# Kernel optimization log

Measured on AMD Instinct MI355X. Metric: run time of the kernel, lower is better.

The kernel has to match this reference:

```python
import jax, jax.numpy as jnp
import numpy as np

# Topology constants for size='large'
S = 490          # total switches: 128+64+64+96+64+32+32+10
W = 64           # n_wavelengths
M = 32           # n_modes
PS = 4           # patch_size
NPATCH = 49      # 7x7 patches of a 28x28 image
V1_START = 0
OUT_START = 480  # OUT region = last 10 switches
OUT_COUNT = 10
N_CLASSES = 10
SAT = 1.0        # cfg.saturation (not shown in source; standard value)
DECAY = 0.15
EPS = 1e-8


def encode_batch(images):
    """Real-valued patch encoding: [B,28,28] -> [B,49,64,32]."""
    B = images.shape[0]
    # unfold into non-overlapping 4x4 patches
    p = images[:, :7 * PS, :7 * PS].reshape(B, 7, PS, 7, PS)
    p = p.transpose(0, 1, 3, 2, 4).reshape(B, NPATCH, PS * PS)
    p = jnp.pad(p, ((0, 0), (0, 0), (0, M - PS * PS)))  # pad 16 -> 32 modes
    w_idx = jnp.arange(W, dtype=jnp.float32)
    w_weights = 1.0 - jnp.abs(w_idx - 32.0) / 64.0      # [W]
    return p[:, :, None, :] * w_weights[None, None, :, None]  # [B,NP,W,M]


def setup_inputs() -> dict:
    key = jax.random.key(0)
    k = jax.random.split(key, 7)
    images = jax.random.uniform(k[0], (8, 28, 28), dtype=jnp.float32)
    connectivity = jax.random.normal(k[1], (S, S), dtype=jnp.float32) * 0.05
    wavelength_weights = jax.random.uniform(k[2], (S, W), dtype=jnp.float32)
    switch_gain = jax.random.normal(k[3], (S,), dtype=jnp.float32) * 0.1
    switch_bias = jax.random.normal(k[4], (S,), dtype=jnp.float32) * 0.1
    readout_w = jax.random.normal(k[5], (N_CLASSES, OUT_COUNT), dtype=jnp.float32) * 0.1
    readout_b = jnp.zeros((N_CLASSES,), dtype=jnp.float32)
    return {
        "images": images,
        "connectivity": connectivity,
        "wavelength_weights": wavelength_weights,
        "switch_gain": switch_gain,
        "switch_bias": switch_bias,
        "readout_w": readout_w,
        "readout_b": readout_b,
        "n_steps": 15,
        "injection_steps": 5,
    }


def reference(images, connectivity, wavelength_weights, switch_gain, switch_bias,
              readout_w, readout_b, n_steps, injection_steps):
    B = images.shape[0]
    enc = encode_batch(images)                          # [B,49,W,M]
    enc_max = jnp.max(jnp.abs(enc))
    enc = jnp.where(enc_max > EPS, enc / enc_max, enc)
    inj = enc * 0.3                                     # injected signal (real; imag part is 0)

    gain = jax.nn.softplus(switch_gain)[None, :, None, None]
    bias = switch_bias[None, :, None, None]
    ww = wavelength_weights[None, :, :, None]

    field = jnp.zeros((B, S, W, M), jnp.float32)
    output = jnp.zeros((B, S, W, M), jnp.float32)

    def step(carry, t):
        field, output = carry
        # injection into V1 (min(v1_count=128, 49 patches) = 49) for t < injection_steps
        gate = jnp.where(t < injection_steps, 1.0, 0.0).astype(jnp.float32)
        field = field.at[:, V1_START:V1_START + NPATCH].add(gate * inj)
        # network step (complex magnitudes; imag is identically 0)
        out_mag = jnp.sqrt(output * output + EPS)
        gathered = jax.nn.relu(jnp.einsum('bswm,st->btwm', out_mag, connectivity))
        field_mag = jnp.sqrt(field * field + EPS) * (1.0 - DECAY) + gathered * 0.25
        weighted = field_mag * ww
        activated = SAT * jnp.tanh((weighted * gain + bias) / SAT)
        return (field_mag, activated), None

    (field, output), _ = jax.lax.scan(step, (field, output), jnp.arange(n_steps))

    out_field = output[:, OUT_START:OUT_START + OUT_COUNT]       # [B,10,W,M]
    out_energy = (out_field * out_field + EPS).sum(axis=(2, 3))  # [B,10]
    out_features = jnp.log1p(out_energy + EPS)
    return out_features @ readout_w.T + readout_b
```

## Files before the change

kernel.cpp:

```cpp
#include <hip/hip_runtime.h>
#include <math.h>

#define S_DIM 490
#define NPATCH 49
#define EPSF 1e-8f
#define SP 512
#define CI 8192
#define CPB 32
#define NBLK 256
#define HEAVY0 252
#define OMS 520

typedef __attribute__((ext_vector_type(8))) short bf16x8;
typedef __attribute__((ext_vector_type(4))) float f32x4;

__device__ __forceinline__ unsigned short f2bf(float x) {
    unsigned int u = __float_as_uint(x);
    unsigned int r = (u + 0x7FFF + ((u >> 16) & 1)) >> 16;
    return (unsigned short)r;
}
__device__ __forceinline__ float bf2f(unsigned short u) {
    return __uint_as_float(((unsigned int)u) << 16);
}

__global__ void k_max(const float* __restrict__ img, float* __restrict__ encmax) {
    __shared__ float red[256];
    float m = 0.f;
    for (int i = threadIdx.x; i < 8 * 28 * 28; i += 256)
        m = fmaxf(m, fabsf(img[i]));
    red[threadIdx.x] = m;
    __syncthreads();
    for (int s = 128; s > 0; s >>= 1) {
        if (threadIdx.x < s) red[threadIdx.x] = fmaxf(red[threadIdx.x], red[threadIdx.x + s]);
        __syncthreads();
    }
    if (threadIdx.x == 0) *encmax = red[0];
}

__global__ void k_prep(const float* __restrict__ ww, const float* __restrict__ sg,
                       const float* __restrict__ sb, float* __restrict__ K1,
                       float* __restrict__ K2) {
    int i = blockIdx.x * 256 + threadIdx.x;
    if (i < 64 * SP) {
        int w = i >> 9, t = i & (SP - 1);
        K1[i] = (t < S_DIM) ? ww[t * 64 + w] * log1pf(expf(sg[t])) : 0.f;
    }
    if (i < SP) K2[i] = (i < S_DIM) ? sb[i] : 0.f;
}

__global__ void k_connP(const float* __restrict__ conn, unsigned short* __restrict__ connP) {
    int i = blockIdx.x * 256 + threadIdx.x;
    int j    = i & 7;
    int lane = (i >> 3) & 63;
    int k    = (i >> 9) & 15;
    int tt   = (i >> 13) & 1;
    int strip = i >> 14;
    int t = strip * 32 + tt * 16 + (lane & 15);
    int s = k * 32 + (lane >> 4) * 8 + j;
    float v = (t < S_DIM && s < S_DIM) ? conn[s * S_DIM + t] : 0.f;
    connP[i] = f2bf(v);
}

__global__ void k_inj(const float* __restrict__ img, const float* __restrict__ encmax,
                      float* __restrict__ injT) {
    int i = blockIdx.x * 256 + threadIdx.x;
    int c = i >> 6, tt = i & 63;
    int b = c >> 10, w = (c >> 4) & 63, m = c & 15;
    float em = *encmax;
    float scale = (em > EPSF) ? (0.3f / em) : 0.3f;
    float v = 0.f;
    if (tt < NPATCH) {
        int r = (tt / 7) * 4 + (m >> 2);
        int col = (tt % 7) * 4 + (m & 3);
        float wgt = 1.0f - fabsf((float)w - 32.0f) * (1.0f / 64.0f);
        v = img[(b * 28 + r) * 28 + col] * wgt * scale;
    }
    injT[i] = v;
}

#define MFMA(A, B, C) __builtin_amdgcn_mfma_f32_16x16x32_bf16(A, B, C, 0, 0, 0)

__global__ __launch_bounds__(1024, 4) void k_run(
    const unsigned short* __restrict__ connP, const float* __restrict__ injT,
    const float* __restrict__ K1, const float* __restrict__ K2,
    const int* __restrict__ injSteps, float* __restrict__ partials,
    float* __restrict__ partialsS)
{
    __shared__ unsigned short om[48 * OMS];
    const int bk   = blockIdx.x;
    const int tid  = threadIdx.x;
    const int wv   = tid >> 6;
    const int lane = tid & 63;
    const int l16  = lane & 15, lq = lane >> 4;
    const bool heavy = (bk >= HEAVY0);
    const int c0 = bk * CPB;

    {
        const unsigned short iv = f2bf(1e-4f);
        for (int i = tid; i < 48 * OMS; i += 1024) om[i] = iv;
    }

    const int nInj = injSteps[0];
    const unsigned short* aP = connP + (size_t)(wv * 32) * 512 + lane * 8;

    f32x4 k1r[2][2], k2r[2], k1h[2];
    #pragma unroll
    for (int tt = 0; tt < 2; ++tt) {
        int t0 = (wv << 5) + tt * 16 + lq * 4;
        k2r[tt] = *(const f32x4*)(K2 + t0);
        #pragma unroll
        for (int cc = 0; cc < 2; ++cc) {
            int w = (2 * bk + cc) & 63;
            k1r[tt][cc] = *(const f32x4*)(K1 + w * SP + t0);
        }
        if (heavy) {
            int wsh = (bk - HEAVY0) * 16 + l16;
            k1h[tt] = *(const f32x4*)(K1 + wsh * SP + t0);
        }
    }

    const int rb0 = l16 * OMS;
    const int rb1 = (16 + l16) * OMS;
    const int rb2 = (32 + l16) * OMS;

    f32x4 fld[2][2] = {};
    f32x4 fld2[2] = {};
    __syncthreads();

    for (int st = 0; st < 15; ++st) {
        f32x4 acc[2][2] = {};
        f32x4 acc2[2] = {};
        __builtin_amdgcn_s_setprio(1);
        #pragma unroll 4
        for (int k = 0; k < 16; ++k) {
            bf16x8 a0 = *(const bf16x8*)(aP + (size_t)(k)      * 512);
            bf16x8 a1 = *(const bf16x8*)(aP + (size_t)(16 + k) * 512);
            int sOff = k * 32 + lq * 8;
            bf16x8 b0 = *(const bf16x8*)&om[rb0 + sOff];
            bf16x8 b1 = *(const bf16x8*)&om[rb1 + sOff];
            acc[0][0] = MFMA(a0, b0, acc[0][0]);
            acc[0][1] = MFMA(a0, b1, acc[0][1]);
            acc[1][0] = MFMA(a1, b0, acc[1][0]);
            acc[1][1] = MFMA(a1, b1, acc[1][1]);
            if (heavy) {
                bf16x8 b2 = *(const bf16x8*)&om[rb2 + sOff];
                acc2[0] = MFMA(a0, b2, acc2[0]);
                acc2[1] = MFMA(a1, b2, acc2[1]);
            }
        }
        __builtin_amdgcn_s_setprio(0);
        __syncthreads();

        const bool injNow = (wv < 2) && (st < nInj);
        #pragma unroll
        for (int tt = 0; tt < 2; ++tt) {
            int t0 = (wv << 5) + tt * 16 + lq * 4;
            f32x4 k2 = k2r[tt];
            #pragma unroll
            for (int cc = 0; cc < 2; ++cc) {
                int cg = c0 + cc * 16 + l16;
                f32x4 k1 = k1r[tt][cc];
                f32x4 f = fld[tt][cc];
                if (injNow) f += *(const f32x4*)(injT + (size_t)cg * 64 + t0);
                f32x4 ac = acc[tt][cc];
                float o_[4];
                #pragma unroll
                for (int r = 0; r < 4; ++r) {
                    float g  = fmaxf(ac[r], 0.f);
                    float fm = fabsf(f[r]) * 0.85f + 0.25f * g;
                    float x  = fabsf(fm * k1[r] + k2[r]);
                    float e  = exp2f(x * 2.8853900817779268f);
                    o_[r] = 1.f - 2.f * __builtin_amdgcn_rcpf(e + 1.f);
                    f[r] = fm;
                }
                fld[tt][cc] = f;
                unsigned int r01, r23;
                asm("v_cvt_pk_bf16_f32 %0, %1, %2" : "=v"(r01) : "v"(o_[0]), "v"(o_[1]));
                asm("v_cvt_pk_bf16_f32 %0, %1, %2" : "=v"(r23) : "v"(o_[2]), "v"(o_[3]));
                int cl = cc * 16 + l16;
                *(uint2*)&om[cl * OMS + t0] = make_uint2(r01, r23);
            }
            if (heavy) {
                f32x4 k1 = k1h[tt];
                f32x4 fh = fld2[tt];
                f32x4 ah = acc2[tt];
                float oh[4];
                #pragma unroll
                for (int r = 0; r < 4; ++r) {
                    float g  = fmaxf(ah[r], 0.f);
                    float fm = fabsf(fh[r]) * 0.85f + 0.25f * g;
                    float x  = fabsf(fm * k1[r] + k2[r]);
                    float e  = exp2f(x * 2.8853900817779268f);
                    oh[r] = 1.f - 2.f * __builtin_amdgcn_rcpf(e + 1.f);
                    fh[r] = fm;
                }
                fld2[tt] = fh;
                unsigned int h01, h23;
                asm("v_cvt_pk_bf16_f32 %0, %1, %2" : "=v"(h01) : "v"(oh[0]), "v"(oh[1]));
                asm("v_cvt_pk_bf16_f32 %0, %1, %2" : "=v"(h23) : "v"(oh[2]), "v"(oh[3]));
                *(uint2*)&om[(32 + l16) * OMS + t0] = make_uint2(h01, h23);
            }
        }
        __syncthreads();
    }

    if (wv == 0) {
        int cl = (lane < 48) ? lane : 0;
        #pragma unroll
        for (int o = 0; o < 10; ++o) {
            float v = bf2f(om[cl * OMS + 480 + o]);
            float e = v * v;
            float em = (lane < 32) ? e : 0.f;
            em += __shfl_xor(em, 1);  em += __shfl_xor(em, 2);
            em += __shfl_xor(em, 4);  em += __shfl_xor(em, 8);
            em += __shfl_xor(em, 16);
            if (lane == 0) partials[bk * 10 + o] = em;
            if (heavy) {
                float es = (lane >= 32 && lane < 48) ? e : 0.f;
                es += __shfl_xor(es, 1); es += __shfl_xor(es, 2);
                es += __shfl_xor(es, 4); es += __shfl_xor(es, 8);
                if (lane == 32) partialsS[(bk - HEAVY0) * 10 + o] = es;
            }
        }
    }
}

__global__ void k_fin(const float* __restrict__ partials, const float* __restrict__ partialsS,
                      const float* __restrict__ rw, const float* __restrict__ rb,
                      float* __restrict__ out) {
    __shared__ float fe[80];
    int tid = threadIdx.x;
    if (tid < 80) {
        int b = tid / 10, o = tid % 10;
        float e = 0.f;
        #pragma unroll 8
        for (int j = 0; j < 32; ++j) e += partials[(b * 32 + j) * 10 + o];
        float es = 0.f;
        #pragma unroll
        for (int j = 0; j < 4; ++j) es += partialsS[j * 10 + o];
        e += 16.f * es + 2048.f * EPSF;
        fe[tid] = log1pf(e + EPSF);
    }
    __syncthreads();
    if (tid < 80) {
        int b = tid / 10, cls = tid % 10;
        float a = rb[cls];
        #pragma unroll
        for (int k = 0; k < 10; ++k) a += fe[b * 10 + k] * rw[cls * 10 + k];
        out[tid] = a;
    }
}

extern "C" void kernel_launch(void* const* d_in, const int* in_sizes, int n_in,
                              void* d_out, int out_size, void* d_ws, size_t ws_size,
                              hipStream_t stream) {
    (void)in_sizes; (void)n_in; (void)out_size; (void)ws_size;
    const float* img   = (const float*)d_in[0];
    const float* conn  = (const float*)d_in[1];
    const float* ww    = (const float*)d_in[2];
    const float* sgain = (const float*)d_in[3];
    const float* sbias = (const float*)d_in[4];
    const float* rw    = (const float*)d_in[5];
    const float* rb    = (const float*)d_in[6];
    const int* injsteps = (const int*)d_in[8];

    char* w = (char*)d_ws;
    unsigned short* connP = (unsigned short*)w;
    float* injT = (float*)(w + (size_t)SP * SP * 2);
    float* K1   = injT + (size_t)CI * 64;
    float* K2   = K1 + 64 * SP;
    float* encmax    = K2 + SP;
    float* partials  = encmax + 4;
    float* partialsS = partials + NBLK * 10;

    k_max  <<<1, 256, 0, stream>>>(img, encmax);
    k_prep <<<128, 256, 0, stream>>>(ww, sgain, sbias, K1, K2);
    k_connP<<<(SP * SP) / 256, 256, 0, stream>>>(conn, connP);
    k_inj  <<<(CI * 64) / 256, 256, 0, stream>>>(img, encmax, injT);

    k_run<<<NBLK, 1024, 0, stream>>>(connP, injT, K1, K2, injsteps, partials, partialsS);
    k_fin<<<1, 128, 0, stream>>>(partials, partialsS, rw, rb, (float*)d_out);
}
```

Before: 135.7 us.

## Double-buffer LDS state to drop a barrier and preload half of connectivity

Doubles the shared output buffer so each step reads one buffer and writes the other, which removes the barrier between the MFMA phase and the activation phase. It also keeps the first eight k-slices of the connectivity A-operand in registers across all steps, avoiding repeated global loads for them. In exchange, LDS use and VGPR pressure both roughly double, which risks spills or lower occupancy.

```diff
diff --git a/kernel.cpp b/kernel.cpp
--- a/kernel.cpp
+++ b/kernel.cpp
@@ -86,7 +86,7 @@
     const int* __restrict__ injSteps, float* __restrict__ partials,
     float* __restrict__ partialsS)
 {
-    __shared__ unsigned short om[48 * OMS];
+    __shared__ unsigned short om[2][48 * OMS];
     const int bk   = blockIdx.x;
     const int tid  = threadIdx.x;
     const int wv   = tid >> 6;
@@ -97,11 +97,18 @@
 
     {
         const unsigned short iv = f2bf(1e-4f);
-        for (int i = tid; i < 48 * OMS; i += 1024) om[i] = iv;
+        for (int i = tid; i < 2 * 48 * OMS; i += 1024) ((unsigned short*)om)[i] = iv;
     }
 
     const int nInj = injSteps[0];
     const unsigned short* aP = connP + (size_t)(wv * 32) * 512 + lane * 8;
+
+    bf16x8 pa0[8], pa1[8];
+    #pragma unroll
+    for (int k = 0; k < 8; ++k) {
+        pa0[k] = *(const bf16x8*)(aP + (size_t)(k)      * 512);
+        pa1[k] = *(const bf16x8*)(aP + (size_t)(16 + k) * 512);
+    }
 
     f32x4 k1r[2][2], k2r[2], k1h[2];
     #pragma unroll
@@ -128,28 +135,44 @@
     __syncthreads();
 
     for (int st = 0; st < 15; ++st) {
+        const unsigned short* bufR = om[st & 1];
+        unsigned short* bufW = om[(st + 1) & 1];
         f32x4 acc[2][2] = {};
         f32x4 acc2[2] = {};
         __builtin_amdgcn_s_setprio(1);
-        #pragma unroll 4
-        for (int k = 0; k < 16; ++k) {
+        #pragma unroll
+        for (int k = 0; k < 8; ++k) {
+            int sOff = k * 32 + lq * 8;
+            bf16x8 b0 = *(const bf16x8*)&bufR[rb0 + sOff];
+            bf16x8 b1 = *(const bf16x8*)&bufR[rb1 + sOff];
+            acc[0][0] = MFMA(pa0[k], b0, acc[0][0]);
+            acc[0][1] = MFMA(pa0[k], b1, acc[0][1]);
+            acc[1][0] = MFMA(pa1[k], b0, acc[1][0]);
+            acc[1][1] = MFMA(pa1[k], b1, acc[1][1]);
+            if (heavy) {
+                bf16x8 b2 = *(const bf16x8*)&bufR[rb2 + sOff];
+                acc2[0] = MFMA(pa0[k], b2, acc2[0]);
+                acc2[1] = MFMA(pa1[k], b2, acc2[1]);
+            }
+        }
+        #pragma unroll
+        for (int k = 8; k < 16; ++k) {
             bf16x8 a0 = *(const bf16x8*)(aP + (size_t)(k)      * 512);
             bf16x8 a1 = *(const bf16x8*)(aP + (size_t)(16 + k) * 512);
             int sOff = k * 32 + lq * 8;
-            bf16x8 b0 = *(const bf16x8*)&om[rb0 + sOff];
-            bf16x8 b1 = *(const bf16x8*)&om[rb1 + sOff];
+            bf16x8 b0 = *(const bf16x8*)&bufR[rb0 + sOff];
+            bf16x8 b1 = *(const bf16x8*)&bufR[rb1 + sOff];
             acc[0][0] = MFMA(a0, b0, acc[0][0]);
             acc[0][1] = MFMA(a0, b1, acc[0][1]);
             acc[1][0] = MFMA(a1, b0, acc[1][0]);
             acc[1][1] = MFMA(a1, b1, acc[1][1]);
             if (heavy) {
-                bf16x8 b2 = *(const bf16x8*)&om[rb2 + sOff];
+                bf16x8 b2 = *(const bf16x8*)&bufR[rb2 + sOff];
                 acc2[0] = MFMA(a0, b2, acc2[0]);
                 acc2[1] = MFMA(a1, b2, acc2[1]);
             }
         }
         __builtin_amdgcn_s_setprio(0);
-        __syncthreads();
 
         const bool injNow = (wv < 2) && (st < nInj);
         #pragma unroll
@@ -178,7 +201,7 @@
                 asm("v_cvt_pk_bf16_f32 %0, %1, %2" : "=v"(r01) : "v"(o_[0]), "v"(o_[1]));
                 asm("v_cvt_pk_bf16_f32 %0, %1, %2" : "=v"(r23) : "v"(o_[2]), "v"(o_[3]));
                 int cl = cc * 16 + l16;
-                *(uint2*)&om[cl * OMS + t0] = make_uint2(r01, r23);
+                *(uint2*)&bufW[cl * OMS + t0] = make_uint2(r01, r23);
             }
             if (heavy) {
                 f32x4 k1 = k1h[tt];
@@ -198,7 +221,7 @@
                 unsigned int h01, h23;
                 asm("v_cvt_pk_bf16_f32 %0, %1, %2" : "=v"(h01) : "v"(oh[0]), "v"(oh[1]));
                 asm("v_cvt_pk_bf16_f32 %0, %1, %2" : "=v"(h23) : "v"(oh[2]), "v"(oh[3]));
-                *(uint2*)&om[(32 + l16) * OMS + t0] = make_uint2(h01, h23);
+                *(uint2*)&bufW[(32 + l16) * OMS + t0] = make_uint2(h01, h23);
             }
         }
         __syncthreads();
@@ -208,7 +231,7 @@
         int cl = (lane < 48) ? lane : 0;
         #pragma unroll
         for (int o = 0; o < 10; ++o) {
-            float v = bf2f(om[cl * OMS + 480 + o]);
+            float v = bf2f(om[1][cl * OMS + 480 + o]);
             float e = v * v;
             float em = (lane < 32) ? e : 0.f;
             em += __shfl_xor(em, 1);  em += __shfl_xor(em, 2);
```

Measured after the change: 327.3 us. 2.41x slower.
